# Kernel tuning notes

Hardware: AMD Instinct MI355X
Metric: run time of the kernel (lower is better)

Reference implementation:

```python
import jax, jax.numpy as jnp
import numpy as np

N = 100000
E = 1600000
D_IN = 128
D_H = 128
D_OUT = 64
HEADS = 8
CH = D_H // HEADS  # 16
LRELU_SLOPE = 0.2
LN_EPS = 1e-5


def setup_inputs() -> dict:
    key = jax.random.key(0)
    ks = jax.random.split(key, 20)
    g = lambda k, shp, scale: (jax.random.normal(k, shp, jnp.float32) * scale)
    return {
        "x": jax.random.normal(ks[0], (N, D_IN), jnp.float32),
        "edge_index": jax.random.randint(ks[1], (2, E), 0, N, dtype=jnp.int32),
        # conv0: in 128 -> 8 heads x 16
        "W0": g(ks[2], (D_IN, HEADS * CH), 0.1),
        "as0": g(ks[3], (HEADS, CH), 0.1),
        "ad0": g(ks[4], (HEADS, CH), 0.1),
        "b0": jnp.zeros((HEADS * CH,), jnp.float32),
        # conv1: 128 -> 8 heads x 16
        "W1": g(ks[5], (D_H, HEADS * CH), 0.1),
        "as1": g(ks[6], (HEADS, CH), 0.1),
        "ad1": g(ks[7], (HEADS, CH), 0.1),
        "b1": jnp.zeros((HEADS * CH,), jnp.float32),
        # conv2 (last): 128 -> 1 head x 64, concat
        "W2": g(ks[8], (D_H, D_OUT), 0.1),
        "as2": g(ks[9], (1, D_OUT), 0.1),
        "ad2": g(ks[10], (1, D_OUT), 0.1),
        "b2": jnp.zeros((D_OUT,), jnp.float32),
        # LayerNorms applied after conv0 and conv1 (lns[1], lns[2]; lns[0] unused)
        "ln1_g": jnp.ones((D_H,), jnp.float32),
        "ln1_b": jnp.zeros((D_H,), jnp.float32),
        "ln2_g": jnp.ones((D_H,), jnp.float32),
        "ln2_b": jnp.zeros((D_H,), jnp.float32),
    }


def _layer_norm(x, gamma, beta):
    mu = jnp.mean(x, axis=-1, keepdims=True)
    var = jnp.mean((x - mu) ** 2, axis=-1, keepdims=True)
    return (x - mu) * jax.lax.rsqrt(var + LN_EPS) * gamma + beta


def _gat_conv(x, src, dst, W, a_src, a_dst, bias, heads, ch):
    n = x.shape[0]
    h = (x @ W).reshape(n, heads, ch)                 # [N,H,C]
    als = jnp.sum(h * a_src, axis=-1)                 # [N,H]
    ald = jnp.sum(h * a_dst, axis=-1)                 # [N,H]
    e = jax.nn.leaky_relu(als[src] + ald[dst], LRELU_SLOPE)   # [E',H]
    emax = jax.ops.segment_max(e, dst, num_segments=n)        # [N,H]
    ee = jnp.exp(e - emax[dst])
    denom = jax.ops.segment_sum(ee, dst, num_segments=n)      # [N,H]
    alpha = ee / denom[dst]                                    # [E',H]
    out = jax.ops.segment_sum(h[src] * alpha[:, :, None], dst, num_segments=n)
    return out.reshape(n, heads * ch) + bias


def reference(x, edge_index, W0, as0, ad0, b0, W1, as1, ad1, b1,
              W2, as2, ad2, b2, ln1_g, ln1_b, ln2_g, ln2_b):
    n = x.shape[0]
    loops = jnp.arange(n, dtype=edge_index.dtype)
    src = jnp.concatenate([edge_index[0], loops])  # PyG add_self_loops=True
    dst = jnp.concatenate([edge_index[1], loops])

    h = _gat_conv(x, src, dst, W0, as0, ad0, b0, HEADS, CH)
    h = jax.nn.relu(_layer_norm(h, ln1_g, ln1_b))   # dropout is identity in eval

    h = _gat_conv(h, src, dst, W1, as1, ad1, b1, HEADS, CH)
    h = jax.nn.relu(_layer_norm(h, ln2_g, ln2_b))

    h = _gat_conv(h, src, dst, W2, as2, ad2, b2, 1, D_OUT)
    return jax.nn.log_softmax(h, axis=-1)
```

## Files before the change

kernel.cpp:

```cpp
#include <hip/hip_runtime.h>


#define LRELU_SLOPE 0.2f
#define LN_EPS 1e-5f
typedef unsigned int u32;
typedef unsigned short u16;
typedef unsigned char u8;
typedef float f32x2 __attribute__((ext_vector_type(2)));
typedef float f32x4 __attribute__((ext_vector_type(4)));
typedef short bf16x8 __attribute__((ext_vector_type(8)));

__device__ __forceinline__ u16 f2bf(float f) {
  u32 u = __float_as_uint(f);
  return (u16)((u + 0x7FFFu + ((u >> 16) & 1u)) >> 16);
}
__device__ __forceinline__ float bf1(u16 w) { return __uint_as_float((u32)w << 16); }

__global__ void wcvt_kernel(const float* __restrict__ W0,
                            const float* __restrict__ W1,
                            const float* __restrict__ W2,
                            u16* __restrict__ Wt0, u16* __restrict__ Wt1,
                            u16* __restrict__ Wt2, u32* __restrict__ deg, int n) {
  int i = blockIdx.x * 256 + threadIdx.x;
  if (i < 16384) {
    int k = i >> 7, c = i & 127;
    Wt0[c * 128 + k] = f2bf(W0[i]);
  } else if (i < 32768) {
    int j = i - 16384;
    int k = j >> 7, c = j & 127;
    Wt1[c * 128 + k] = f2bf(W1[j]);
  } else if (i < 40960) {
    int j = i - 32768;
    int k = j >> 6, c = j & 63;
    Wt2[c * 128 + k] = f2bf(W2[j]);
  }
  for (int j = i; j < n; j += 40960) deg[j] = 0u;
}

template <int DOUT, int NH, bool XBF, bool F8OUT>
__global__ __launch_bounds__(256) void feat_mfma(
    const void* __restrict__ Xv, const u16* __restrict__ Wtg,
    const float* __restrict__ As, const float* __restrict__ Ad,
    u16* __restrict__ HfB, u8* __restrict__ Hf8,
    float* __restrict__ als, float* __restrict__ ald, int n) {
  constexpr int NT = DOUT / 16;
  constexpr int XP = 136;
  __shared__ u16 Wl[DOUT * XP];
  __shared__ u16 Xl[64 * XP];
  __shared__ float AsL[DOUT], AdL[DOUT];

  const int tid = threadIdx.x;
  const int base = blockIdx.x * 64;

  if (tid < DOUT) { AsL[tid] = As[tid]; AdL[tid] = Ad[tid]; }
  for (int i = tid; i < DOUT * 16; i += 256) {
    int c = i >> 4, k0 = (i & 15) * 8;
    *(uint4*)&Wl[c * XP + k0] = *(const uint4*)&Wtg[c * 128 + k0];
  }
  for (int i = tid; i < 64 * 16; i += 256) {
    int r = i >> 4, k0 = (i & 15) * 8;
    int node = base + r;
    uint4 o = uint4{0, 0, 0, 0};
    if (node < n) {
      if (XBF) {
        o = *(const uint4*)((const u16*)Xv + (size_t)node * 128 + k0);
      } else {
        const float* Xf = (const float*)Xv;
        float4 v0 = *(const float4*)&Xf[(size_t)node * 128 + k0];
        float4 v1 = *(const float4*)&Xf[(size_t)node * 128 + k0 + 4];
        o.x = (u32)f2bf(v0.x) | ((u32)f2bf(v0.y) << 16);
        o.y = (u32)f2bf(v0.z) | ((u32)f2bf(v0.w) << 16);
        o.z = (u32)f2bf(v1.x) | ((u32)f2bf(v1.y) << 16);
        o.w = (u32)f2bf(v1.z) | ((u32)f2bf(v1.w) << 16);
      }
    }
    *(uint4*)&Xl[r * XP + k0] = o;
  }
  __syncthreads();

  const int w = tid >> 6, l = tid & 63;
  const int lr = l & 15, lg = l >> 4;
  f32x4 acc[NT];
#pragma unroll
  for (int t = 0; t < NT; ++t) acc[t] = f32x4{0.f, 0.f, 0.f, 0.f};

#pragma unroll
  for (int ks = 0; ks < 4; ++ks) {
    int kb = ks * 32 + lg * 8;
    bf16x8 a = *(const bf16x8*)&Xl[(w * 16 + lr) * XP + kb];
#pragma unroll
    for (int t = 0; t < NT; ++t) {
      bf16x8 b = *(const bf16x8*)&Wl[(t * 16 + lr) * XP + kb];
      acc[t] = __builtin_amdgcn_mfma_f32_16x16x32_bf16(a, b, acc[t], 0, 0, 0);
    }
  }

#pragma unroll
  for (int t = 0; t < NT; ++t)
#pragma unroll
    for (int j = 0; j < 4; ++j)
      Xl[(w * 16 + lg * 4 + j) * XP + t * 16 + lr] = f2bf(acc[t][j]);
  __syncthreads();

  if (F8OUT) {
    for (int i = tid; i < 64 * (DOUT / 8); i += 256) {
      int r = i / (DOUT / 8), c0 = (i % (DOUT / 8)) * 8;
      int node = base + r;
      if (node < n) {
        float f[8];
#pragma unroll
        for (int j = 0; j < 8; ++j) f[j] = bf1(Xl[r * XP + c0 + j]);
        int lo = 0, hi = 0;
        lo = __builtin_amdgcn_cvt_pk_fp8_f32(f[0], f[1], lo, false);
        lo = __builtin_amdgcn_cvt_pk_fp8_f32(f[2], f[3], lo, true);
        hi = __builtin_amdgcn_cvt_pk_fp8_f32(f[4], f[5], hi, false);
        hi = __builtin_amdgcn_cvt_pk_fp8_f32(f[6], f[7], hi, true);
        uint2 o = {(u32)lo, (u32)hi};
        *(uint2*)&Hf8[(size_t)node * DOUT + c0] = o;
      }
    }
  } else {
    for (int i = tid; i < 64 * (DOUT / 8); i += 256) {
      int r = i / (DOUT / 8), k0 = (i % (DOUT / 8)) * 8;
      int node = base + r;
      if (node < n)
        *(uint4*)&HfB[(size_t)node * DOUT + k0] = *(const uint4*)&Xl[r * XP + k0];
    }
  }

  int row = tid >> 2, quad = tid & 3;
  int node = base + row;
  if (NH == 8) {
#pragma unroll
    for (int h2 = 0; h2 < 2; ++h2) {
      int h = quad * 2 + h2;
      float ps = 0.f, pd = 0.f;
#pragma unroll
      for (int i2 = 0; i2 < 16; ++i2) {
        float hv = bf1(Xl[row * XP + h * 16 + i2]);
        ps = fmaf(hv, AsL[h * 16 + i2], ps);
        pd = fmaf(hv, AdL[h * 16 + i2], pd);
      }
      if (node < n) {
        als[node * 8 + h] = ps;
        ald[node * 8 + h] = pd;
      }
    }
  } else {
    float ps = 0.f, pd = 0.f;
#pragma unroll
    for (int i2 = 0; i2 < 16; ++i2) {
      float hv = bf1(Xl[row * XP + quad * 16 + i2]);
      ps = fmaf(hv, AsL[quad * 16 + i2], ps);
      pd = fmaf(hv, AdL[quad * 16 + i2], pd);
    }
    ps += __shfl_xor(ps, 1, 64);
    ps += __shfl_xor(ps, 2, 64);
    pd += __shfl_xor(pd, 1, 64);
    pd += __shfl_xor(pd, 2, 64);
    if (quad == 0 && node < n) {
      als[node] = ps;
      ald[node] = pd;
    }
  }
}

__global__ __launch_bounds__(256) void deg_kernel(
    const int* __restrict__ ei, u32* __restrict__ deg, int E, int n,
    int nper, int chunk) {
  const int lo = (blockIdx.x & 7) * nper;
  const int hi = min(lo + nper, n);
  const int e0 = (blockIdx.x >> 3) * chunk;
  const int e1 = min(e0 + chunk, E + n);
  for (int e = e0 + (int)threadIdx.x; e < e1; e += 256) {
    int d = (e < E) ? ei[E + e] : (e - E);
    if (d >= lo && d < hi) atomicAdd(&deg[d], 1u);
  }
}

__global__ __launch_bounds__(1024) void scan1_kernel(const u32* __restrict__ deg,
                                                     u32* __restrict__ offs,
                                                     u32* __restrict__ bsum, int n) {
  __shared__ u32 tmp[1024];
  int t = threadIdx.x, i = blockIdx.x * 1024 + t;
  u32 v = (i < n) ? deg[i] : 0u;
  tmp[t] = v;
  __syncthreads();
  for (int off = 1; off < 1024; off <<= 1) {
    u32 a = (t >= off) ? tmp[t - off] : 0u;
    __syncthreads();
    tmp[t] += a;
    __syncthreads();
  }
  if (i < n) offs[i] = tmp[t] - v;
  if (t == 1023) bsum[blockIdx.x] = tmp[t];
}

__global__ __launch_bounds__(1024) void scan23_kernel(
    u32* __restrict__ offs, const u32* __restrict__ bsum,
    u32* __restrict__ cursor, int n, u32 total, int nb) {
  __shared__ u32 tmp[1024];
  int t = threadIdx.x;
  tmp[t] = (t < nb && t < (int)blockIdx.x) ? bsum[t] : 0u;
  __syncthreads();
#pragma unroll
  for (int off = 512; off > 0; off >>= 1) {
    if (t < off) tmp[t] += tmp[t + off];
    __syncthreads();
  }
  u32 prefix = tmp[0];
  int i = blockIdx.x * 1024 + t;
  if (i < n) {
    u32 v = offs[i] + prefix;
    offs[i] = v;
    cursor[i] = v;
  }
  if (i == 0) offs[n] = total;
}

__global__ __launch_bounds__(256) void fill_kernel(
    const int* __restrict__ ei, u32* __restrict__ cursor,
    int* __restrict__ csr_src, int E, int n, int nper, int chunk) {
  const int lo = (blockIdx.x & 7) * nper;
  const int hi = min(lo + nper, n);
  const int e0 = (blockIdx.x >> 3) * chunk;
  const int e1 = min(e0 + chunk, E + n);
  for (int e = e0 + (int)threadIdx.x; e < e1; e += 256) {
    int d = (e < E) ? ei[E + e] : (e - E);
    if (d >= lo && d < hi) {
      int s = (e < E) ? ei[e] : d;
      u32 pos = atomicAdd(&cursor[d], 1u);
      csr_src[pos] = s;
    }
  }
}

__global__ __launch_bounds__(256) void gat_gather128(
    const u32* __restrict__ offs, const int* __restrict__ csr,
    const float* __restrict__ als, const float* __restrict__ ald,
    const u8* __restrict__ Hf8, const float* __restrict__ bias,
    const float* __restrict__ g, const float* __restrict__ b,
    u16* __restrict__ outp, int n) {
  int d = blockIdx.x * 4 + (threadIdx.x >> 6);
  if (d >= n) return;
  const int lane = threadIdx.x & 63;
  const int h = lane >> 3;
  const float adv = ald[d * 8 + h];
  const u16* HfP = (const u16*)Hf8;
  f32x2 acc2 = {0.f, 0.f};
  float lsum = 0.f;

  u32 k0 = offs[d], k1 = offs[d + 1], k = k0;
  for (; k + 8 <= k1; k += 8) {
    int s[8];
#pragma unroll
    for (int i = 0; i < 8; ++i) s[i] = csr[k + i];
    u16 w[8];
#pragma unroll
    for (int i = 0; i < 8; ++i) w[i] = HfP[(u32)s[i] * 64 + lane];
    int smine = csr[k + (lane & 7)];
    float v = als[smine * 8 + h] + adv;
    v = fmaxf(v, LRELU_SLOPE * v);
    float pm = __expf(v);
#pragma unroll
    for (int i = 0; i < 8; ++i) {
      float p = __shfl(pm, i, 8);
      lsum += p;
      f32x2 hw = __builtin_amdgcn_cvt_pk_f32_fp8((int)w[i], false);
      f32x2 pv = {p, p};
      acc2 = pv * hw + acc2;
    }
  }
  if (k + 4 <= k1) {
    int s[4];
    float a[4];
    u16 w[4];
#pragma unroll
    for (int i = 0; i < 4; ++i) s[i] = csr[k + i];
#pragma unroll
    for (int i = 0; i < 4; ++i) {
      a[i] = als[s[i] * 8 + h];
      w[i] = HfP[(u32)s[i] * 64 + lane];
    }
#pragma unroll
    for (int i = 0; i < 4; ++i) {
      float v = a[i] + adv;
      v = fmaxf(v, LRELU_SLOPE * v);
      float p = __expf(v);
      lsum += p;
      f32x2 hw = __builtin_amdgcn_cvt_pk_f32_fp8((int)w[i], false);
      f32x2 pv = {p, p};
      acc2 = pv * hw + acc2;
    }
    k += 4;
  }
  for (; k < k1; ++k) {
    int s = csr[k];
    float aa = als[s * 8 + h];
    u16 w = HfP[(u32)s * 64 + lane];
    float v = aa + adv;
    v = fmaxf(v, LRELU_SLOPE * v);
    float p = __expf(v);
    lsum += p;
    f32x2 hw = __builtin_amdgcn_cvt_pk_f32_fp8((int)w, false);
    f32x2 pv = {p, p};
    acc2 = pv * hw + acc2;
  }

  float inv = 1.f / lsum;
  float2 bs = *(const float2*)&bias[2 * lane];
  float r0 = acc2.x * inv + bs.x, r1 = acc2.y * inv + bs.y;
  float ssum = r0 + r1;
#pragma unroll
  for (int off = 32; off > 0; off >>= 1) ssum += __shfl_xor(ssum, off, 64);
  float mu = ssum * (1.f / 128.f);
  float d0 = r0 - mu, d1 = r1 - mu;
  float q = d0 * d0 + d1 * d1;
#pragma unroll
  for (int off = 32; off > 0; off >>= 1) q += __shfl_xor(q, off, 64);
  float rstd = rsqrtf(q * (1.f / 128.f) + LN_EPS);
  float2 gg = *(const float2*)&g[2 * lane];
  float2 bb = *(const float2*)&b[2 * lane];
  float o0 = fmaxf(d0 * rstd * gg.x + bb.x, 0.f);
  float o1 = fmaxf(d1 * rstd * gg.y + bb.y, 0.f);
  u32 packed = (u32)f2bf(o0) | ((u32)f2bf(o1) << 16);
  *(u32*)&outp[(size_t)d * 128 + 2 * lane] = packed;
}

__global__ __launch_bounds__(256) void gat_gather64(
    const u32* __restrict__ offs, const int* __restrict__ csr,
    const float* __restrict__ als, const float* __restrict__ ald,
    const u16* __restrict__ HfB, const float* __restrict__ bias,
    float* __restrict__ outp, int n) {
  int d = blockIdx.x * 4 + (threadIdx.x >> 6);
  if (d >= n) return;
  const int lane = threadIdx.x & 63;
  const float adv = ald[d];
  float acc = 0.f, lsum = 0.f;
  u32 k0 = offs[d], k1 = offs[d + 1], k = k0;
  for (; k + 8 <= k1; k += 8) {
    int s[8];
#pragma unroll
    for (int i = 0; i < 8; ++i) s[i] = csr[k + i];
    u16 w[8];
#pragma unroll
    for (int i = 0; i < 8; ++i) w[i] = HfB[(size_t)s[i] * 64 + lane];
    int smine = csr[k + (lane & 7)];
    float v = als[smine] + adv;
    v = fmaxf(v, LRELU_SLOPE * v);
    float pm = __expf(v);
#pragma unroll
    for (int i = 0; i < 8; ++i) {
      float p = __shfl(pm, i, 8);
      lsum += p;
      acc = fmaf(p, bf1(w[i]), acc);
    }
  }
  if (k + 4 <= k1) {
    int s[4];
    float a[4];
    u16 w[4];
#pragma unroll
    for (int i = 0; i < 4; ++i) s[i] = csr[k + i];
#pragma unroll
    for (int i = 0; i < 4; ++i) {
      a[i] = als[s[i]];
      w[i] = HfB[(size_t)s[i] * 64 + lane];
    }
#pragma unroll
    for (int i = 0; i < 4; ++i) {
      float v = a[i] + adv;
      v = fmaxf(v, LRELU_SLOPE * v);
      float p = __expf(v);
      lsum += p;
      acc = fmaf(p, bf1(w[i]), acc);
    }
    k += 4;
  }
  for (; k < k1; ++k) {
    int s = csr[k];
    float v = als[s] + adv;
    v = fmaxf(v, LRELU_SLOPE * v);
    float p = __expf(v);
    lsum += p;
    acc = fmaf(p, bf1(HfB[(size_t)s * 64 + lane]), acc);
  }
  float v = acc / lsum + bias[lane];
  float mx = v;
#pragma unroll
  for (int off = 32; off > 0; off >>= 1) mx = fmaxf(mx, __shfl_xor(mx, off, 64));
  float e = __expf(v - mx);
  float ssum = e;
#pragma unroll
  for (int off = 32; off > 0; off >>= 1) ssum += __shfl_xor(ssum, off, 64);
  outp[(size_t)d * 64 + lane] = v - mx - __logf(ssum);
}

extern "C" void kernel_launch(void* const* d_in, const int* in_sizes, int n_in,
                              void* d_out, int out_size, void* d_ws,
                              size_t ws_size, hipStream_t stream) {
  const float* x    = (const float*)d_in[0];
  const int*   ei   = (const int*)d_in[1];
  const float* W0   = (const float*)d_in[2];
  const float* as0  = (const float*)d_in[3];
  const float* ad0  = (const float*)d_in[4];
  const float* b0   = (const float*)d_in[5];
  const float* W1   = (const float*)d_in[6];
  const float* as1  = (const float*)d_in[7];
  const float* ad1  = (const float*)d_in[8];
  const float* b1   = (const float*)d_in[9];
  const float* W2   = (const float*)d_in[10];
  const float* as2  = (const float*)d_in[11];
  const float* ad2  = (const float*)d_in[12];
  const float* b2   = (const float*)d_in[13];
  const float* ln1g = (const float*)d_in[14];
  const float* ln1b = (const float*)d_in[15];
  const float* ln2g = (const float*)d_in[16];
  const float* ln2b = (const float*)d_in[17];

  const int n = in_sizes[0] / 128;
  const int E = in_sizes[1] / 2;
  const int EP = E + n;

  u16* bufXb = (u16*)d_ws;
  u16* HfB   = bufXb + (size_t)n * 128;
  u8*  Hf8   = (u8*)(HfB + (size_t)n * 128);
  u16* Wt0   = (u16*)(Hf8 + (size_t)n * 128);
  u16* Wt1   = Wt0 + 16384;
  u16* Wt2   = Wt1 + 16384;
  float* als = (float*)(Wt2 + 8192);
  float* ald = als + (size_t)n * 8;
  u32* deg    = (u32*)(ald + (size_t)n * 8);
  u32* offs   = deg + n;
  u32* cursor = offs + (n + 1);
  u32* bsum   = cursor + n;
  int* csr    = (int*)(bsum + 1024);

  const dim3 blk(256);
  const int gFeat = (n + 63) / 64;
  const int gGath = (n + 3) / 4;
  const int nb = (n + 1023) / 1024;
  const int SEGS = 256;
  const int nper = (n + 7) / 8;
  const int chunk = (EP + SEGS - 1) / SEGS;

  wcvt_kernel<<<160, blk, 0, stream>>>(W0, W1, W2, Wt0, Wt1, Wt2, deg, n);
  deg_kernel<<<8 * SEGS, blk, 0, stream>>>(ei, deg, E, n, nper, chunk);
  scan1_kernel<<<nb, 1024, 0, stream>>>(deg, offs, bsum, n);
  scan23_kernel<<<nb, 1024, 0, stream>>>(offs, bsum, cursor, n, (u32)EP, nb);
  fill_kernel<<<8 * SEGS, blk, 0, stream>>>(ei, cursor, csr, E, n, nper, chunk);

  feat_mfma<128, 8, false, true><<<gFeat, blk, 0, stream>>>(
      x, Wt0, as0, ad0, HfB, Hf8, als, ald, n);
  gat_gather128<<<gGath, blk, 0, stream>>>(
      offs, csr, als, ald, Hf8, b0, ln1g, ln1b, bufXb, n);

  feat_mfma<128, 8, true, true><<<gFeat, blk, 0, stream>>>(
      bufXb, Wt1, as1, ad1, HfB, Hf8, als, ald, n);
  gat_gather128<<<gGath, blk, 0, stream>>>(
      offs, csr, als, ald, Hf8, b1, ln2g, ln2b, bufXb, n);

  feat_mfma<64, 1, true, false><<<gFeat, blk, 0, stream>>>(
      bufXb, Wt2, as2, ad2, HfB, Hf8, als, ald, n);
  gat_gather64<<<gGath, blk, 0, stream>>>(
      offs, csr, als, ald, HfB, b2, (float*)d_out, n);
}
```

Before: 523.8 us.

## Use half-wave per node in gathers and precompute edge ranks for CSR fill

The CSR build now records each edge's atomic rank during a single-pass degree count, and the fill kernel writes to offs[d]+rank[e] with no second atomic pass, so the cursor array goes away. Both gather kernels now give each destination node 32 lanes instead of 64. Each lane loads a 32-bit word (4 fp8 or 2 bf16 values), which halves wave usage per node and widens the loads. The trade-offs are a flat, unpartitioned atomic pass over all edges, which may hurt atomic locality, and an extra rank array of E+N entries to write and read.

```diff
diff --git a/kernel.cpp b/kernel.cpp
--- a/kernel.cpp
+++ b/kernel.cpp
@@ -14,6 +14,8 @@
   u32 u = __float_as_uint(f);
   return (u16)((u + 0x7FFFu + ((u >> 16) & 1u)) >> 16);
 }
+__device__ __forceinline__ float bflo(u32 w) { return __uint_as_float(w << 16); }
+__device__ __forceinline__ float bfhi(u32 w) { return __uint_as_float(w & 0xFFFF0000u); }
 __device__ __forceinline__ float bf1(u16 w) { return __uint_as_float((u32)w << 16); }
 
 __global__ void wcvt_kernel(const float* __restrict__ W0,
@@ -165,17 +167,12 @@
   }
 }
 
-__global__ __launch_bounds__(256) void deg_kernel(
-    const int* __restrict__ ei, u32* __restrict__ deg, int E, int n,
-    int nper, int chunk) {
-  const int lo = (blockIdx.x & 7) * nper;
-  const int hi = min(lo + nper, n);
-  const int e0 = (blockIdx.x >> 3) * chunk;
-  const int e1 = min(e0 + chunk, E + n);
-  for (int e = e0 + (int)threadIdx.x; e < e1; e += 256) {
-    int d = (e < E) ? ei[E + e] : (e - E);
-    if (d >= lo && d < hi) atomicAdd(&deg[d], 1u);
-  }
+__global__ void deg_kernel(const int* __restrict__ ei, u32* __restrict__ deg,
+                           u32* __restrict__ rank, int E, int n) {
+  int e = blockIdx.x * blockDim.x + threadIdx.x;
+  if (e >= E + n) return;
+  int d = (e < E) ? ei[E + e] : (e - E);
+  rank[e] = atomicAdd(&deg[d], 1u);
 }
 
 __global__ __launch_bounds__(1024) void scan1_kernel(const u32* __restrict__ deg,
@@ -197,8 +194,8 @@
 }
 
 __global__ __launch_bounds__(1024) void scan23_kernel(
-    u32* __restrict__ offs, const u32* __restrict__ bsum,
-    u32* __restrict__ cursor, int n, u32 total, int nb) {
+    u32* __restrict__ offs, const u32* __restrict__ bsum, int n, u32 total,
+    int nb) {
   __shared__ u32 tmp[1024];
   int t = threadIdx.x;
   tmp[t] = (t < nb && t < (int)blockIdx.x) ? bsum[t] : 0u;
@@ -210,17 +207,14 @@
   }
   u32 prefix = tmp[0];
   int i = blockIdx.x * 1024 + t;
-  if (i < n) {
-    u32 v = offs[i] + prefix;
-    offs[i] = v;
-    cursor[i] = v;
-  }
+  if (i < n) offs[i] += prefix;
   if (i == 0) offs[n] = total;
 }
 
 __global__ __launch_bounds__(256) void fill_kernel(
-    const int* __restrict__ ei, u32* __restrict__ cursor,
-    int* __restrict__ csr_src, int E, int n, int nper, int chunk) {
+    const int* __restrict__ ei, const u32* __restrict__ offs,
+    const u32* __restrict__ rank, int* __restrict__ csr_src, int E, int n,
+    int nper, int chunk) {
   const int lo = (blockIdx.x & 7) * nper;
   const int hi = min(lo + nper, n);
   const int e0 = (blockIdx.x >> 3) * chunk;
@@ -229,8 +223,7 @@
     int d = (e < E) ? ei[E + e] : (e - E);
     if (d >= lo && d < hi) {
       int s = (e < E) ? ei[e] : d;
-      u32 pos = atomicAdd(&cursor[d], 1u);
-      csr_src[pos] = s;
+      csr_src[offs[d] + rank[e]] = s;
     }
   }
 }
@@ -241,13 +234,14 @@
     const u8* __restrict__ Hf8, const float* __restrict__ bias,
     const float* __restrict__ g, const float* __restrict__ b,
     u16* __restrict__ outp, int n) {
-  int d = blockIdx.x * 4 + (threadIdx.x >> 6);
+  int d = blockIdx.x * 8 + (threadIdx.x >> 5);
   if (d >= n) return;
-  const int lane = threadIdx.x & 63;
-  const int h = lane >> 3;
+  const int l = threadIdx.x & 31;
+  const int h = l >> 2;
+  const int jgrp = l & 3;
   const float adv = ald[d * 8 + h];
-  const u16* HfP = (const u16*)Hf8;
-  f32x2 acc2 = {0.f, 0.f};
+  const u32* HfW = (const u32*)Hf8;
+  f32x2 accA = {0.f, 0.f}, accB = {0.f, 0.f};
   float lsum = 0.f;
 
   u32 k0 = offs[d], k1 = offs[d + 1], k = k0;
@@ -255,76 +249,81 @@
     int s[8];
 #pragma unroll
     for (int i = 0; i < 8; ++i) s[i] = csr[k + i];
-    u16 w[8];
-#pragma unroll
-    for (int i = 0; i < 8; ++i) w[i] = HfP[(u32)s[i] * 64 + lane];
-    int smine = csr[k + (lane & 7)];
-    float v = als[smine * 8 + h] + adv;
-    v = fmaxf(v, LRELU_SLOPE * v);
-    float pm = __expf(v);
+    u32 w[8];
+#pragma unroll
+    for (int i = 0; i < 8; ++i) w[i] = HfW[(u32)s[i] * 32 + l];
+    int sA = csr[k + 2 * jgrp];
+    int sB = csr[k + 2 * jgrp + 1];
+    float vA = als[sA * 8 + h] + adv;
+    vA = fmaxf(vA, LRELU_SLOPE * vA);
+    float pA = __expf(vA);
+    float vB = als[sB * 8 + h] + adv;
+    vB = fmaxf(vB, LRELU_SLOPE * vB);
+    float pB = __expf(vB);
 #pragma unroll
     for (int i = 0; i < 8; ++i) {
-      float p = __shfl(pm, i, 8);
+      float p = __shfl((i & 1) ? pB : pA, i >> 1, 4);
       lsum += p;
-      f32x2 hw = __builtin_amdgcn_cvt_pk_f32_fp8((int)w[i], false);
       f32x2 pv = {p, p};
-      acc2 = pv * hw + acc2;
+      accA = pv * __builtin_amdgcn_cvt_pk_f32_fp8((int)w[i], false) + accA;
+      accB = pv * __builtin_amdgcn_cvt_pk_f32_fp8((int)w[i], true) + accB;
     }
   }
   if (k + 4 <= k1) {
     int s[4];
-    float a[4];
-    u16 w[4];
 #pragma unroll
     for (int i = 0; i < 4; ++i) s[i] = csr[k + i];
+    u32 w[4];
+#pragma unroll
+    for (int i = 0; i < 4; ++i) w[i] = HfW[(u32)s[i] * 32 + l];
+    int sA = csr[k + jgrp];
+    float vA = als[sA * 8 + h] + adv;
+    vA = fmaxf(vA, LRELU_SLOPE * vA);
+    float pA = __expf(vA);
 #pragma unroll
     for (int i = 0; i < 4; ++i) {
-      a[i] = als[s[i] * 8 + h];
-      w[i] = HfP[(u32)s[i] * 64 + lane];
-    }
-#pragma unroll
-    for (int i = 0; i < 4; ++i) {
-      float v = a[i] + adv;
-      v = fmaxf(v, LRELU_SLOPE * v);
-      float p = __expf(v);
+      float p = __shfl(pA, i, 4);
       lsum += p;
-      f32x2 hw = __builtin_amdgcn_cvt_pk_f32_fp8((int)w[i], false);
       f32x2 pv = {p, p};
-      acc2 = pv * hw + acc2;
+      accA = pv * __builtin_amdgcn_cvt_pk_f32_fp8((int)w[i], false) + accA;
+      accB = pv * __builtin_amdgcn_cvt_pk_f32_fp8((int)w[i], true) + accB;
     }
     k += 4;
   }
   for (; k < k1; ++k) {
     int s = csr[k];
-    float aa = als[s * 8 + h];
-    u16 w = HfP[(u32)s * 64 + lane];
-    float v = aa + adv;
+    float v = als[s * 8 + h] + adv;
     v = fmaxf(v, LRELU_SLOPE * v);
     float p = __expf(v);
+    u32 w = HfW[(u32)s * 32 + l];
     lsum += p;
-    f32x2 hw = __builtin_amdgcn_cvt_pk_f32_fp8((int)w, false);
     f32x2 pv = {p, p};
-    acc2 = pv * hw + acc2;
+    accA = pv * __builtin_amdgcn_cvt_pk_f32_fp8((int)w, false) + accA;
+    accB = pv * __builtin_amdgcn_cvt_pk_f32_fp8((int)w, true) + accB;
   }
 
   float inv = 1.f / lsum;
-  float2 bs = *(const float2*)&bias[2 * lane];
-  float r0 = acc2.x * inv + bs.x, r1 = acc2.y * inv + bs.y;
-  float ssum = r0 + r1;
-#pragma unroll
-  for (int off = 32; off > 0; off >>= 1) ssum += __shfl_xor(ssum, off, 64);
+  float4 bs = *(const float4*)&bias[4 * l];
+  float r0 = accA.x * inv + bs.x, r1 = accA.y * inv + bs.y;
+  float r2 = accB.x * inv + bs.z, r3 = accB.y * inv + bs.w;
+  float ssum = r0 + r1 + r2 + r3;
+#pragma unroll
+  for (int off = 16; off > 0; off >>= 1) ssum += __shfl_xor(ssum, off, 32);
   float mu = ssum * (1.f / 128.f);
-  float d0 = r0 - mu, d1 = r1 - mu;
-  float q = d0 * d0 + d1 * d1;
-#pragma unroll
-  for (int off = 32; off > 0; off >>= 1) q += __shfl_xor(q, off, 64);
+  float d0 = r0 - mu, d1 = r1 - mu, d2 = r2 - mu, d3 = r3 - mu;
+  float q = d0 * d0 + d1 * d1 + d2 * d2 + d3 * d3;
+#pragma unroll
+  for (int off = 16; off > 0; off >>= 1) q += __shfl_xor(q, off, 32);
   float rstd = rsqrtf(q * (1.f / 128.f) + LN_EPS);
-  float2 gg = *(const float2*)&g[2 * lane];
-  float2 bb = *(const float2*)&b[2 * lane];
+  float4 gg = *(const float4*)&g[4 * l];
+  float4 bb = *(const float4*)&b[4 * l];
   float o0 = fmaxf(d0 * rstd * gg.x + bb.x, 0.f);
   float o1 = fmaxf(d1 * rstd * gg.y + bb.y, 0.f);
-  u32 packed = (u32)f2bf(o0) | ((u32)f2bf(o1) << 16);
-  *(u32*)&outp[(size_t)d * 128 + 2 * lane] = packed;
+  float o2 = fmaxf(d2 * rstd * gg.z + bb.z, 0.f);
+  float o3 = fmaxf(d3 * rstd * gg.w + bb.w, 0.f);
+  uint2 packed = {(u32)f2bf(o0) | ((u32)f2bf(o1) << 16),
+                  (u32)f2bf(o2) | ((u32)f2bf(o3) << 16)};
+  *(uint2*)&outp[(size_t)d * 128 + 4 * l] = packed;
 }
 
 __global__ __launch_bounds__(256) void gat_gather64(
@@ -332,48 +331,52 @@
     const float* __restrict__ als, const float* __restrict__ ald,
     const u16* __restrict__ HfB, const float* __restrict__ bias,
     float* __restrict__ outp, int n) {
-  int d = blockIdx.x * 4 + (threadIdx.x >> 6);
+  int d = blockIdx.x * 8 + (threadIdx.x >> 5);
   if (d >= n) return;
-  const int lane = threadIdx.x & 63;
+  const int l = threadIdx.x & 31;
   const float adv = ald[d];
-  float acc = 0.f, lsum = 0.f;
+  const u32* HfW = (const u32*)HfB;
+  f32x2 acc2 = {0.f, 0.f};
+  float lsum = 0.f;
   u32 k0 = offs[d], k1 = offs[d + 1], k = k0;
   for (; k + 8 <= k1; k += 8) {
     int s[8];
 #pragma unroll
     for (int i = 0; i < 8; ++i) s[i] = csr[k + i];
-    u16 w[8];
-#pragma unroll
-    for (int i = 0; i < 8; ++i) w[i] = HfB[(size_t)s[i] * 64 + lane];
-    int smine = csr[k + (lane & 7)];
-    float v = als[smine] + adv;
+    u32 w[8];
+#pragma unroll
+    for (int i = 0; i < 8; ++i) w[i] = HfW[(u32)s[i] * 32 + l];
+    int sm = csr[k + (l & 7)];
+    float v = als[sm] + adv;
     v = fmaxf(v, LRELU_SLOPE * v);
     float pm = __expf(v);
 #pragma unroll
     for (int i = 0; i < 8; ++i) {
       float p = __shfl(pm, i, 8);
       lsum += p;
-      acc = fmaf(p, bf1(w[i]), acc);
+      f32x2 hw = {bflo(w[i]), bfhi(w[i])};
+      f32x2 pv = {p, p};
+      acc2 = pv * hw + acc2;
     }
   }
   if (k + 4 <= k1) {
     int s[4];
-    float a[4];
-    u16 w[4];
 #pragma unroll
     for (int i = 0; i < 4; ++i) s[i] = csr[k + i];
+    u32 w[4];
+#pragma unroll
+    for (int i = 0; i < 4; ++i) w[i] = HfW[(u32)s[i] * 32 + l];
+    int sm = csr[k + (l & 3)];
+    float v = als[sm] + adv;
+    v = fmaxf(v, LRELU_SLOPE * v);
+    float pm = __expf(v);
 #pragma unroll
     for (int i = 0; i < 4; ++i) {
-      a[i] = als[s[i]];
-      w[i] = HfB[(size_t)s[i] * 64 + lane];
-    }
-#pragma unroll
-    for (int i = 0; i < 4; ++i) {
-      float v = a[i] + adv;
-      v = fmaxf(v, LRELU_SLOPE * v);
-      float p = __expf(v);
+      float p = __shfl(pm, i, 4);
       lsum += p;
-      acc = fmaf(p, bf1(w[i]), acc);
+      f32x2 hw = {bflo(w[i]), bfhi(w[i])};
+      f32x2 pv = {p, p};
+      acc2 = pv * hw + acc2;
     }
     k += 4;
   }
@@ -382,18 +385,24 @@
     float v = als[s] + adv;
     v = fmaxf(v, LRELU_SLOPE * v);
     float p = __expf(v);
+    u32 w = HfW[(u32)s * 32 + l];
     lsum += p;
-    acc = fmaf(p, bf1(HfB[(size_t)s * 64 + lane]), acc);
-  }
-  float v = acc / lsum + bias[lane];
-  float mx = v;
-#pragma unroll
-  for (int off = 32; off > 0; off >>= 1) mx = fmaxf(mx, __shfl_xor(mx, off, 64));
-  float e = __expf(v - mx);
-  float ssum = e;
-#pragma unroll
-  for (int off = 32; off > 0; off >>= 1) ssum += __shfl_xor(ssum, off, 64);
-  outp[(size_t)d * 64 + lane] = v - mx - __logf(ssum);
+    f32x2 hw = {bflo(w), bfhi(w)};
+    f32x2 pv = {p, p};
+    acc2 = pv * hw + acc2;
+  }
+  float inv = 1.f / lsum;
+  float2 bs = *(const float2*)&bias[2 * l];
+  float r0 = acc2.x * inv + bs.x, r1 = acc2.y * inv + bs.y;
+  float mx = fmaxf(r0, r1);
+#pragma unroll
+  for (int off = 16; off > 0; off >>= 1) mx = fmaxf(mx, __shfl_xor(mx, off, 32));
+  float e = __expf(r0 - mx) + __expf(r1 - mx);
+#pragma unroll
+  for (int off = 16; off > 0; off >>= 1) e += __shfl_xor(e, off, 32);
+  float lse = __logf(e);
+  *(float2*)&outp[(size_t)d * 64 + 2 * l] =
+      float2{r0 - mx - lse, r1 - mx - lse};
 }
 
 extern "C" void kernel_launch(void* const* d_in, const int* in_sizes, int n_in,
@@ -430,25 +439,26 @@
   u16* Wt2   = Wt1 + 16384;
   float* als = (float*)(Wt2 + 8192);
   float* ald = als + (size_t)n * 8;
-  u32* deg    = (u32*)(ald + (size_t)n * 8);
-  u32* offs   = deg + n;
-  u32* cursor = offs + (n + 1);
-  u32* bsum   = cursor + n;
-  int* csr    = (int*)(bsum + 1024);
+  u32* deg   = (u32*)(ald + (size_t)n * 8);
+  u32* offs  = deg + n;
+  u32* bsum  = offs + (n + 1);
+  int* csr   = (int*)(bsum + 1024);
+  u32* rank  = (u32*)(csr + EP);
 
   const dim3 blk(256);
   const int gFeat = (n + 63) / 64;
-  const int gGath = (n + 3) / 4;
+  const int gGath = (n + 7) / 8;
+  const int gEdge = (EP + 255) / 256;
   const int nb = (n + 1023) / 1024;
   const int SEGS = 256;
   const int nper = (n + 7) / 8;
   const int chunk = (EP + SEGS - 1) / SEGS;
 
   wcvt_kernel<<<160, blk, 0, stream>>>(W0, W1, W2, Wt0, Wt1, Wt2, deg, n);
-  deg_kernel<<<8 * SEGS, blk, 0, stream>>>(ei, deg, E, n, nper, chunk);
+  deg_kernel<<<gEdge, blk, 0, stream>>>(ei, deg, rank, E, n);
   scan1_kernel<<<nb, 1024, 0, stream>>>(deg, offs, bsum, n);
-  scan23_kernel<<<nb, 1024, 0, stream>>>(offs, bsum, cursor, n, (u32)EP, nb);
-  fill_kernel<<<8 * SEGS, blk, 0, stream>>>(ei, cursor, csr, E, n, nper, chunk);
+  scan23_kernel<<<nb, 1024, 0, stream>>>(offs, bsum, n, (u32)EP, nb);
+  fill_kernel<<<8 * SEGS, blk, 0, stream>>>(ei, offs, rank, csr, E, n, nper, chunk);
 
   feat_mfma<128, 8, false, true><<<gFeat, blk, 0, stream>>>(
       x, Wt0, as0, ad0, HfB, Hf8, als, ald, n);
```

Result: faster. 432.1 us (-17.5%).
